# Optimization experiments

Hardware: AMD Instinct MI355X
Metric: run time of the kernel (lower is better)

Reference implementation:

```python
import jax, jax.numpy as jnp
import numpy as np

B, N, OBS, ACT, HID, GD, H = 1024, 64, 128, 16, 256, 64, 4
NEG_SLOPE = 0.2  # GAT leaky-relu alpha


def _gat(x, adj, W, a, concat):
    # x: (B,N,F), W: (H,F,D), a: (H,2D). Equivalent to concat([x_i,x_j]) . a
    # split as x_i.a1 + x_j.a2 -- same math, avoids the (B,H,N,N,2D) tensor.
    D = W.shape[-1]
    xt = jnp.einsum('bnf,hfd->bhnd', x, W)
    si = jnp.einsum('bhnd,hd->bhn', xt, a[:, :D])
    sj = jnp.einsum('bhnd,hd->bhn', xt, a[:, D:])
    s = jax.nn.leaky_relu(si[:, :, :, None] + sj[:, :, None, :], NEG_SLOPE)
    s = jnp.where(adj[:, None, :, :] == 0, -jnp.inf, s)
    w = jax.nn.softmax(s, axis=-1)
    out = jnp.einsum('bhij,bhjd->bhid', w, xt)
    if concat:
        b, n = x.shape[0], x.shape[1]
        return out.transpose(0, 2, 1, 3).reshape(b, n, -1)
    return out.mean(axis=1)


def _mlp3(x, w1, b1, w2, b2, w3, b3):
    # per-agent 3-layer MLP, weights stacked over agent axis n
    h = jax.nn.relu(jnp.einsum('bni,nih->bnh', x, w1) + b1)
    h = jax.nn.relu(jnp.einsum('bnh,nhk->bnk', h, w2) + b2)
    return jnp.einsum('bnk,nko->bno', h, w3) + b3


def _mlp2(x, w1, b1, w2, b2):
    h = jax.nn.relu(jnp.einsum('bni,nih->bnh', x, w1) + b1)
    return jnp.einsum('bnh,nho->bno', h, w2) + b2


def setup_inputs() -> dict:
    key = jax.random.key(0)
    ks = iter(jax.random.split(key, 64))

    def nrm(shape):
        fan_in = shape[-2] if len(shape) >= 2 else shape[-1]
        return jax.random.normal(next(ks), shape, jnp.float32) * np.float32(1.0 / np.sqrt(fan_in))

    AI = OBS + GD   # actor/critic input dim
    CI = OBS + ACT  # SCM / centralized per-agent input dim
    return dict(
        observations=jax.random.normal(next(ks), (B, N, OBS), jnp.float32),
        actions=jax.random.normal(next(ks), (B, N, ACT), jnp.float32),
        adj_matrix=jnp.ones((B, N, N), jnp.float32),
        causal_structure=jnp.eye(OBS, dtype=jnp.float32),
        gat_W=nrm((H, OBS, GD)), gat_a=nrm((H, 2 * GD)),
        cg_W0=nrm((H, OBS, GD)), cg_a0=nrm((H, 2 * GD)),
        cg_W1=nrm((H, H * GD, GD)), cg_a1=nrm((H, 2 * GD)),
        actor_w1=nrm((N, AI, HID)), actor_b1=jnp.zeros((N, HID), jnp.float32),
        actor_w2=nrm((N, HID, HID)), actor_b2=jnp.zeros((N, HID), jnp.float32),
        actor_w3=nrm((N, HID, ACT)), actor_b3=jnp.zeros((N, ACT), jnp.float32),
        critic_w1=nrm((N, AI, HID)), critic_b1=jnp.zeros((N, HID), jnp.float32),
        critic_w2=nrm((N, HID, HID)), critic_b2=jnp.zeros((N, HID), jnp.float32),
        critic_w3=nrm((N, HID, 1)), critic_b3=jnp.zeros((N, 1), jnp.float32),
        cent_w1=nrm((N * CI, HID)), cent_b1=jnp.zeros((HID,), jnp.float32),
        cent_w2=nrm((HID, HID)), cent_b2=jnp.zeros((HID,), jnp.float32),
        cent_w3=nrm((HID, N)), cent_b3=jnp.zeros((N,), jnp.float32),
        scm_causal=jnp.eye(N, dtype=jnp.float32),
        scm_mw1=nrm((N, CI, HID)), scm_mb1=jnp.zeros((N, HID), jnp.float32),
        scm_mw2=nrm((N, HID, HID)), scm_mb2=jnp.zeros((N, HID), jnp.float32),
        scm_mw3=nrm((N, HID, OBS)), scm_mb3=jnp.zeros((N, OBS), jnp.float32),
        scm_nw1=nrm((N, OBS, HID)), scm_nb1=jnp.zeros((N, HID), jnp.float32),
        scm_nw2=nrm((N, HID, OBS)), scm_nb2=jnp.zeros((N, OBS), jnp.float32),
    )


def reference(observations, actions, adj_matrix, causal_structure,
              gat_W, gat_a, cg_W0, cg_a0, cg_W1, cg_a1,
              actor_w1, actor_b1, actor_w2, actor_b2, actor_w3, actor_b3,
              critic_w1, critic_b1, critic_w2, critic_b2, critic_w3, critic_b3,
              cent_w1, cent_b1, cent_w2, cent_b2, cent_w3, cent_b3,
              scm_causal, scm_mw1, scm_mb1, scm_mw2, scm_mb2, scm_mw3, scm_mb3,
              scm_nw1, scm_nb1, scm_nw2, scm_nb2):
    # plain GAT communication features (concat=False -> head mean)
    gat_feat = _gat(observations, adj_matrix, gat_W, gat_a, False)
    # CausalGAT: causal mask on input features, then 2 GAT layers w/ ELU between
    xm = observations @ jax.nn.softmax(causal_structure, axis=-1)
    hcg = jax.nn.elu(_gat(xm, adj_matrix, cg_W0, cg_a0, True))
    causal_feat = _gat(hcg, adj_matrix, cg_W1, cg_a1, False)
    comm = gat_feat + causal_feat
    ai = jnp.concatenate([observations, comm], axis=-1)  # (B,N,OBS+GD)
    actor_out = _mlp3(ai, actor_w1, actor_b1, actor_w2, actor_b2, actor_w3, actor_b3)
    critic_out = _mlp3(ai, critic_w1, critic_b1, critic_w2, critic_b2, critic_w3, critic_b3)
    # centralized critic over flattened (obs, action) of all agents
    flat = jnp.concatenate([observations, actions], axis=-1).reshape(observations.shape[0], -1)
    hc = jax.nn.relu(flat @ cent_w1 + cent_b1)
    hc = jax.nn.relu(hc @ cent_w2 + cent_b2)
    cent_out = hc @ cent_w3 + cent_b3
    # SCM: per-agent causal mechanisms mixed by softmaxed causal matrix + noise model
    cw = jax.nn.softmax(scm_causal, axis=-1)
    combined = jnp.concatenate([observations, actions], axis=-1)
    ce = _mlp3(combined, scm_mw1, scm_mb1, scm_mw2, scm_mb2, scm_mw3, scm_mb3)
    se = jnp.einsum('ij,bjd->bid', cw, ce)
    noise = _mlp2(observations, scm_nw1, scm_nb1, scm_nw2, scm_nb2)
    scm_pred = se + noise
    return (actor_out, critic_out, cent_out, scm_pred)
```

## Files before the change

kernel.cpp:

```cpp
#include <hip/hip_runtime.h>
#include <hip/hip_bf16.h>
#include <math.h>

#define NB 1024
#define NAG 64
#define OBS 128
#define ACTD 16
#define HID 256
#define GD 64
#define NH 4

typedef short bhalf8 __attribute__((ext_vector_type(8)));
typedef float f32x4 __attribute__((ext_vector_type(4)));

__device__ inline unsigned short f2bf_u(float f) {
  __hip_bfloat16 h = __float2bfloat16(f);
  return *(unsigned short*)&h;
}
__device__ inline float bfu2f(unsigned short u) {
  unsigned v = ((unsigned)u) << 16;
  return *(float*)&v;
}
__device__ inline unsigned pk2(float x, float y) {
  float2 f2; f2.x = x; f2.y = y;
  __hip_bfloat162 h = __float22bfloat162_rn(f2);
  return *(unsigned*)&h;
}

__global__ __launch_bounds__(64) void softmax_rows_k(const float* __restrict__ in,
                                                     float* __restrict__ out, int n) {
  int row = blockIdx.x;
  int lane = threadIdx.x;
  const float* r = in + (size_t)row * n;
  float m = -INFINITY;
  for (int j = lane; j < n; j += 64) m = fmaxf(m, r[j]);
#pragma unroll
  for (int off = 32; off; off >>= 1) m = fmaxf(m, __shfl_xor(m, off));
  float s = 0.f;
  for (int j = lane; j < n; j += 64) s += expf(r[j] - m);
#pragma unroll
  for (int off = 32; off; off >>= 1) s += __shfl_xor(s, off);
  float inv = 1.f / s;
  for (int j = lane; j < n; j += 64) out[(size_t)row * n + j] = expf(r[j] - m) * inv;
}

__global__ void cwbf_k(const float* __restrict__ cwsm, unsigned short* __restrict__ cw1,
                       unsigned short* __restrict__ cw2) {
  int idx = blockIdx.x * 256 + threadIdx.x;
  if (idx >= 4096) return;
  float v = cwsm[idx];
  unsigned short hi = f2bf_u(v);
  cw1[idx] = hi;
  cw2[idx] = f2bf_u(v - bfu2f(hi));
}

__global__ __launch_bounds__(256) void transpose_cvt_k(const float* __restrict__ in,
                                                       unsigned short* __restrict__ out,
                                                       int K, int N) {
  __shared__ float t[32][33];
  int k0 = blockIdx.x * 32, n0 = blockIdx.y * 32, z = blockIdx.z;
  int tx = threadIdx.x, ty = threadIdx.y;
  const float* ib = in + (size_t)z * K * N;
  unsigned short* ob = out + (size_t)z * N * K;
#pragma unroll
  for (int i = 0; i < 4; ++i) {
    int k = k0 + ty + 8 * i, n = n0 + tx;
    if (k < K && n < N) t[ty + 8 * i][tx] = ib[(size_t)k * N + n];
  }
  __syncthreads();
#pragma unroll
  for (int i = 0; i < 4; ++i) {
    int n = n0 + ty + 8 * i, k = k0 + tx;
    if (n < N && k < K) ob[(size_t)n * K + k] = f2bf_u(t[tx][ty + 8 * i]);
  }
}

__global__ void repack_wT_k(const float* __restrict__ W, unsigned short* __restrict__ WcT, int F) {
  int idx = blockIdx.x * 256 + threadIdx.x;
  if (idx >= NH * F * 64) return;
  int d = idx & 63;
  int f = (idx >> 6) % F;
  int h = idx / (F * 64);
  WcT[((size_t)(h * 64 + d)) * F + f] = f2bf_u(W[idx]);
}

__global__ __launch_bounds__(256) void gemm_mfma_k(
    const float* __restrict__ A, const unsigned short* __restrict__ BT,
    const float* __restrict__ bias, float* __restrict__ C,
    int M, int N, int K,
    long long lda, long long ldc,
    long long aBS, long long btBS, long long biasBS, long long cBS,
    int act, int kPerSplit) {
  __shared__ unsigned short As[64 * 40];
  __shared__ unsigned short Bs[64 * 40];
  int tid = threadIdx.x;
  int wave = tid >> 6, lane = tid & 63;
  int m0 = blockIdx.x * 64, n0 = blockIdx.y * 64;
  int z = blockIdx.z;
  const float* Ab;
  const unsigned short* Bb;
  const float* biasb = nullptr;
  float* Cb;
  int k_begin, k_end;
  if (kPerSplit > 0) {
    Ab = A; Bb = BT; Cb = C + (long long)z * cBS;
    k_begin = z * kPerSplit;
    k_end = k_begin + kPerSplit;
    if (k_end > K) k_end = K;
  } else {
    Ab = A + (long long)z * aBS;
    Bb = BT + (long long)z * btBS;
    if (bias) biasb = bias + (long long)z * biasBS;
    Cb = C + (long long)z * cBS;
    k_begin = 0; k_end = K;
  }
  int sr = tid >> 2;
  int sk = (tid & 3) * 8;
  int fr = lane & 15;
  int kq = (lane >> 4) * 8;

  f32x4 zf = {0.f, 0.f, 0.f, 0.f};
  f32x4 acc[4] = {zf, zf, zf, zf};

  const unsigned short* bRow = Bb + (long long)(n0 + sr) * K;
  bool bValid = (n0 + sr) < N;
  const float* aRow = Ab + (long long)(m0 + sr) * lda;

  for (int k0 = k_begin; k0 < k_end; k0 += 32) {
    int kk = k0 + sk;
    uint4 aw;
    if (kk + 7 < k_end) {
      const float* ap = aRow + kk;
      float4 v0 = *(const float4*)ap;
      float4 v1 = *(const float4*)(ap + 4);
      aw.x = pk2(v0.x, v0.y); aw.y = pk2(v0.z, v0.w);
      aw.z = pk2(v1.x, v1.y); aw.w = pk2(v1.z, v1.w);
    } else {
      float t[8];
#pragma unroll
      for (int j = 0; j < 8; ++j) t[j] = (kk + j < k_end) ? aRow[kk + j] : 0.f;
      aw.x = pk2(t[0], t[1]); aw.y = pk2(t[2], t[3]);
      aw.z = pk2(t[4], t[5]); aw.w = pk2(t[6], t[7]);
    }
    *(uint4*)&As[sr * 40 + sk] = aw;
    uint4 bw = {0u, 0u, 0u, 0u};
    if (bValid) {
      if (kk + 7 < k_end) {
        bw = *(const uint4*)(bRow + kk);
      } else {
        unsigned short tb[8];
#pragma unroll
        for (int j = 0; j < 8; ++j) tb[j] = (kk + j < k_end) ? bRow[kk + j] : (unsigned short)0;
        bw.x = (unsigned)tb[0] | ((unsigned)tb[1] << 16);
        bw.y = (unsigned)tb[2] | ((unsigned)tb[3] << 16);
        bw.z = (unsigned)tb[4] | ((unsigned)tb[5] << 16);
        bw.w = (unsigned)tb[6] | ((unsigned)tb[7] << 16);
      }
    }
    *(uint4*)&Bs[sr * 40 + sk] = bw;
    __syncthreads();
    bhalf8 af = *(bhalf8*)&As[(16 * wave + fr) * 40 + kq];
#pragma unroll
    for (int t = 0; t < 4; ++t) {
      bhalf8 bf = *(bhalf8*)&Bs[(16 * t + fr) * 40 + kq];
      acc[t] = __builtin_amdgcn_mfma_f32_16x16x32_bf16(af, bf, acc[t], 0, 0, 0);
    }
    __syncthreads();
  }
  int rb = (lane >> 4) * 4;
#pragma unroll
  for (int t = 0; t < 4; ++t) {
    int col = n0 + 16 * t + fr;
    if (col < N) {
      float bv = biasb ? biasb[col] : 0.f;
#pragma unroll
      for (int r = 0; r < 4; ++r) {
        long long row = m0 + 16 * wave + rb + r;
        float v = acc[t][r] + bv;
        if (act == 1) v = fmaxf(v, 0.f);
        Cb[row * ldc + col] = v;
      }
    }
  }
}

__global__ __launch_bounds__(256) void gemm_mfma128_k(
    const float* __restrict__ A, const unsigned short* __restrict__ BT,
    const float* __restrict__ bias, float* __restrict__ C,
    int M, int N, int K,
    long long lda, long long ldc,
    long long aBS, long long btBS, long long biasBS, long long cBS,
    int act, int kPerSplit) {
  __shared__ unsigned short As[128 * 40];
  __shared__ unsigned short Bs[128 * 40];
  int tid = threadIdx.x;
  int wave = tid >> 6, lane = tid & 63;
  int m0 = blockIdx.x * 128, n0 = blockIdx.y * 128;
  int z = blockIdx.z;
  const float* Ab;
  const unsigned short* Bb;
  const float* biasb = nullptr;
  float* Cb;
  int k_begin, k_end;
  if (kPerSplit > 0) {
    Ab = A; Bb = BT; Cb = C + (long long)z * cBS;
    k_begin = z * kPerSplit;
    k_end = k_begin + kPerSplit;
    if (k_end > K) k_end = K;
  } else {
    Ab = A + (long long)z * aBS;
    Bb = BT + (long long)z * btBS;
    if (bias) biasb = bias + (long long)z * biasBS;
    Cb = C + (long long)z * cBS;
    k_begin = 0; k_end = K;
  }
  int sr = tid >> 1;
  int sk = (tid & 1) * 16;
  int mq = (wave >> 1) * 64;
  int nq = (wave & 1) * 64;
  int fr = lane & 15;
  int kq = (lane >> 4) * 8;

  f32x4 zf = {0.f, 0.f, 0.f, 0.f};
  f32x4 acc[4][4];
#pragma unroll
  for (int i = 0; i < 4; ++i)
#pragma unroll
    for (int j = 0; j < 4; ++j) acc[i][j] = zf;

  const float* aRow = Ab + (long long)(m0 + sr) * lda;
  const unsigned short* bRow = Bb + (long long)(n0 + sr) * K;
  bool bValid = (n0 + sr) < N;

  for (int k0 = k_begin; k0 < k_end; k0 += 32) {
    int kk = k0 + sk;
    uint4 aw0, aw1;
    if (kk + 15 < k_end) {
      const float* ap = aRow + kk;
      float4 v0 = *(const float4*)ap;
      float4 v1 = *(const float4*)(ap + 4);
      float4 v2 = *(const float4*)(ap + 8);
      float4 v3 = *(const float4*)(ap + 12);
      aw0.x = pk2(v0.x, v0.y); aw0.y = pk2(v0.z, v0.w);
      aw0.z = pk2(v1.x, v1.y); aw0.w = pk2(v1.z, v1.w);
      aw1.x = pk2(v2.x, v2.y); aw1.y = pk2(v2.z, v2.w);
      aw1.z = pk2(v3.x, v3.y); aw1.w = pk2(v3.z, v3.w);
    } else {
      float t[16];
#pragma unroll
      for (int j = 0; j < 16; ++j) t[j] = (kk + j < k_end) ? aRow[kk + j] : 0.f;
      aw0.x = pk2(t[0], t[1]);   aw0.y = pk2(t[2], t[3]);
      aw0.z = pk2(t[4], t[5]);   aw0.w = pk2(t[6], t[7]);
      aw1.x = pk2(t[8], t[9]);   aw1.y = pk2(t[10], t[11]);
      aw1.z = pk2(t[12], t[13]); aw1.w = pk2(t[14], t[15]);
    }
    *(uint4*)&As[sr * 40 + sk] = aw0;
    *(uint4*)&As[sr * 40 + sk + 8] = aw1;
    uint4 bw0 = {0u, 0u, 0u, 0u}, bw1 = {0u, 0u, 0u, 0u};
    if (bValid) {
      if (kk + 15 < k_end) {
        bw0 = *(const uint4*)(bRow + kk);
        bw1 = *(const uint4*)(bRow + kk + 8);
      } else {
        unsigned short tb[16];
#pragma unroll
        for (int j = 0; j < 16; ++j) tb[j] = (kk + j < k_end) ? bRow[kk + j] : (unsigned short)0;
        bw0.x = (unsigned)tb[0] | ((unsigned)tb[1] << 16);
        bw0.y = (unsigned)tb[2] | ((unsigned)tb[3] << 16);
        bw0.z = (unsigned)tb[4] | ((unsigned)tb[5] << 16);
        bw0.w = (unsigned)tb[6] | ((unsigned)tb[7] << 16);
        bw1.x = (unsigned)tb[8] | ((unsigned)tb[9] << 16);
        bw1.y = (unsigned)tb[10] | ((unsigned)tb[11] << 16);
        bw1.z = (unsigned)tb[12] | ((unsigned)tb[13] << 16);
        bw1.w = (unsigned)tb[14] | ((unsigned)tb[15] << 16);
      }
    }
    *(uint4*)&Bs[sr * 40 + sk] = bw0;
    *(uint4*)&Bs[sr * 40 + sk + 8] = bw1;
    __syncthreads();
    bhalf8 af[4], bf[4];
#pragma unroll
    for (int i = 0; i < 4; ++i) af[i] = *(bhalf8*)&As[(mq + 16 * i + fr) * 40 + kq];
#pragma unroll
    for (int j = 0; j < 4; ++j) bf[j] = *(bhalf8*)&Bs[(nq + 16 * j + fr) * 40 + kq];
#pragma unroll
    for (int i = 0; i < 4; ++i)
#pragma unroll
      for (int j = 0; j < 4; ++j)
        acc[i][j] = __builtin_amdgcn_mfma_f32_16x16x32_bf16(af[i], bf[j], acc[i][j], 0, 0, 0);
    __syncthreads();
  }
  int rb = (lane >> 4) * 4;
#pragma unroll
  for (int j = 0; j < 4; ++j) {
    int col = n0 + nq + 16 * j + fr;
    if (col < N) {
      float bv = biasb ? biasb[col] : 0.f;
#pragma unroll
      for (int i = 0; i < 4; ++i) {
#pragma unroll
        for (int r = 0; r < 4; ++r) {
          long long row = m0 + mq + 16 * i + rb + r;
          float v = acc[i][j][r] + bv;
          if (act == 1) v = fmaxf(v, 0.f);
          Cb[row * ldc + col] = v;
        }
      }
    }
  }
}

__global__ __launch_bounds__(256, 4) void gat_attn4_k(
    const float* __restrict__ xt, const float* __restrict__ a,
    const float* __restrict__ adj, float* __restrict__ out, int mode) {
  int b = blockIdx.x;
  int tid = threadIdx.x;
  int wave = tid >> 6, lane = tid & 63;
  __shared__ unsigned short xT1[64 * 72];
  __shared__ unsigned short xT2[64 * 72];
  __shared__ unsigned short P1[64 * 72];
  __shared__ unsigned short P2[64 * 72];
  __shared__ float si_s[64], sj_s[64];

  const float* adjb = adj + (size_t)b * 4096;
  float adjv[16];
#pragma unroll
  for (int r = 0; r < 16; ++r) adjv[r] = adjb[(size_t)(wave * 16 + r) * 64 + lane];

  int lrow = tid >> 2;
  int cg = tid & 3;
  int fr = lane & 15;
  int kq = (lane >> 4) * 8;
  int ibase = wave * 16;

  bhalf8 ones;
#pragma unroll
  for (int u = 0; u < 8; ++u) ones[u] = (short)0x3F80;

  f32x4 zf = {0.f, 0.f, 0.f, 0.f};
  f32x4 accm[4] = {zf, zf, zf, zf};

  for (int h = 0; h < 4; ++h) {
    const float* xcol = xt + ((size_t)(b * 64 + 16 * wave)) * 256 + h * 64 + lane;
    float v[16];
#pragma unroll
    for (int u = 0; u < 16; ++u) v[u] = xcol[(size_t)u * 256];

    const float* xrow = xt + ((size_t)(b * 64 + lrow)) * 256 + h * 64 + cg * 16;
    const float* ah = a + h * 128;
    float p1 = 0.f, p2 = 0.f;
#pragma unroll
    for (int q = 0; q < 4; ++q) {
      float4 rv = *(const float4*)(xrow + 4 * q);
      int c = cg * 16 + 4 * q;
      p1 += rv.x * ah[c] + rv.y * ah[c + 1] + rv.z * ah[c + 2] + rv.w * ah[c + 3];
      p2 += rv.x * ah[64 + c] + rv.y * ah[64 + c + 1] + rv.z * ah[64 + c + 2] + rv.w * ah[64 + c + 3];
    }
    p1 += __shfl_xor(p1, 1); p1 += __shfl_xor(p1, 2);
    p2 += __shfl_xor(p2, 1); p2 += __shfl_xor(p2, 2);
    if (cg == 0) { si_s[lrow] = p1; sj_s[lrow] = p2; }

    {
      float hf[16];
      uint4 h0, h1, l0, l1;
#pragma unroll
      for (int u = 0; u < 16; ++u) hf[u] = bfu2f(f2bf_u(v[u]));
      h0.x = pk2(hf[0], hf[1]);   h0.y = pk2(hf[2], hf[3]);
      h0.z = pk2(hf[4], hf[5]);   h0.w = pk2(hf[6], hf[7]);
      h1.x = pk2(hf[8], hf[9]);   h1.y = pk2(hf[10], hf[11]);
      h1.z = pk2(hf[12], hf[13]); h1.w = pk2(hf[14], hf[15]);
      l0.x = pk2(v[0] - hf[0], v[1] - hf[1]);     l0.y = pk2(v[2] - hf[2], v[3] - hf[3]);
      l0.z = pk2(v[4] - hf[4], v[5] - hf[5]);     l0.w = pk2(v[6] - hf[6], v[7] - hf[7]);
      l1.x = pk2(v[8] - hf[8], v[9] - hf[9]);     l1.y = pk2(v[10] - hf[10], v[11] - hf[11]);
      l1.z = pk2(v[12] - hf[12], v[13] - hf[13]); l1.w = pk2(v[14] - hf[14], v[15] - hf[15]);
      int base = lane * 72 + 16 * wave;
      *(uint4*)&xT1[base] = h0;
      *(uint4*)&xT1[base + 8] = h1;
      *(uint4*)&xT2[base] = l0;
      *(uint4*)&xT2[base + 8] = l1;
    }
    __syncthreads();

    float sjv = sj_s[lane];
    float maxsj = sjv;
#pragma unroll
    for (int off = 32; off; off >>= 1) maxsj = fmaxf(maxsj, __shfl_xor(maxsj, off));
#pragma unroll
    for (int r = 0; r < 16; ++r) {
      int i = ibase + r;
      float siv = si_s[i];
      float tM = siv + maxsj;
      float Mi = tM > 0.f ? tM : 0.2f * tM;
      float e = siv + sjv;
      e = e > 0.f ? e : 0.2f * e;
      float p = (adjv[r] == 0.f) ? 0.f : expf(e - Mi);
      unsigned short phi = f2bf_u(p);
      P1[i * 72 + lane] = phi;
      P2[i * 72 + lane] = f2bf_u(p - bfu2f(phi));
    }

    bhalf8 a1[2], a2[2];
#pragma unroll
    for (int ks = 0; ks < 2; ++ks) {
      a1[ks] = *(bhalf8*)&P1[(ibase + fr) * 72 + ks * 32 + kq];
      a2[ks] = *(bhalf8*)&P2[(ibase + fr) * 72 + ks * 32 + kq];
    }
    f32x4 accS = zf;
#pragma unroll
    for (int ks = 0; ks < 2; ++ks) {
      accS = __builtin_amdgcn_mfma_f32_16x16x32_bf16(a1[ks], ones, accS, 0, 0, 0);
      accS = __builtin_amdgcn_mfma_f32_16x16x32_bf16(a2[ks], ones, accS, 0, 0, 0);
    }
    f32x4 acc[4] = {zf, zf, zf, zf};
#pragma unroll
    for (int ks = 0; ks < 2; ++ks) {
#pragma unroll
      for (int t = 0; t < 4; ++t) {
        bhalf8 b1 = *(bhalf8*)&xT1[(16 * t + fr) * 72 + ks * 32 + kq];
        bhalf8 b2 = *(bhalf8*)&xT2[(16 * t + fr) * 72 + ks * 32 + kq];
        acc[t] = __builtin_amdgcn_mfma_f32_16x16x32_bf16(a1[ks], b1, acc[t], 0, 0, 0);
        acc[t] = __builtin_amdgcn_mfma_f32_16x16x32_bf16(a1[ks], b2, acc[t], 0, 0, 0);
        acc[t] = __builtin_amdgcn_mfma_f32_16x16x32_bf16(a2[ks], b1, acc[t], 0, 0, 0);
      }
    }
    f32x4 inv;
#pragma unroll
    for (int r = 0; r < 4; ++r) inv[r] = (accS[r] > 0.f) ? 1.f / accS[r] : 0.f;

    int rb = (lane >> 4) * 4;
    if (mode == 2) {
#pragma unroll
      for (int t = 0; t < 4; ++t) {
#pragma unroll
        for (int r = 0; r < 4; ++r) {
          int i = ibase + rb + r;
          float vv = acc[t][r] * inv[r];
          vv = vv > 0.f ? vv : expf(vv) - 1.f;
          out[((size_t)(b * 64 + i)) * 256 + h * 64 + 16 * t + fr] = vv;
        }
      }
    } else {
#pragma unroll
      for (int t = 0; t < 4; ++t)
#pragma unroll
        for (int r = 0; r < 4; ++r) accm[t][r] += 0.25f * acc[t][r] * inv[r];
    }
    __syncthreads();
  }

  if (mode != 2) {
    int rb = (lane >> 4) * 4;
    float* cb = out + (size_t)b * 4096;
#pragma unroll
    for (int t = 0; t < 4; ++t) {
#pragma unroll
      for (int r = 0; r < 4; ++r) {
        int i = ibase + rb + r;
        int col = 16 * t + fr;
        if (mode == 1) cb[i * 64 + col] += accm[t][r];
        else cb[i * 64 + col] = accm[t][r];
      }
    }
  }
}

__global__ void build_ai_k(const float* __restrict__ obs, const float* __restrict__ comm,
                           float* __restrict__ ai) {
  size_t idx = (size_t)blockIdx.x * 256 + threadIdx.x;
  if (idx >= (size_t)NB * NAG * 192) return;
  int c = (int)(idx % 192);
  size_t bn = idx / 192;
  ai[idx] = (c < 128) ? obs[bn * 128 + c] : comm[bn * 64 + (c - 128)];
}

__global__ void build_combined_k(const float* __restrict__ obs, const float* __restrict__ act,
                                 float* __restrict__ cmb) {
  size_t idx = (size_t)blockIdx.x * 256 + threadIdx.x;
  if (idx >= (size_t)NB * NAG * 144) return;
  int c = (int)(idx % 144);
  size_t bn = idx / 144;
  cmb[idx] = (c < 128) ? obs[bn * 128 + c] : act[bn * 16 + (c - 128)];
}

__global__ void reduce_bias_relu_k(const float* __restrict__ part, const float* __restrict__ bias,
                                   float* __restrict__ out) {
  int idx = blockIdx.x * 256 + threadIdx.x;
  float s = 0.f;
#pragma unroll
  for (int zz = 0; zz < 16; ++zz) s += part[(size_t)zz * 262144 + idx];
  s += bias[idx & 255];
  out[idx] = fmaxf(s, 0.f);
}

__global__ __launch_bounds__(256, 4) void se_noise_mfma_k(
    const unsigned short* __restrict__ cw1, const unsigned short* __restrict__ cw2,
    const float* __restrict__ ce, const float* __restrict__ nz,
    float* __restrict__ out) {
  int b = blockIdx.x;
  int tid = threadIdx.x;
  int wave = tid >> 6, lane = tid & 63;
  __shared__ unsigned short xT1[128 * 72];
  __shared__ unsigned short xT2[128 * 72];

  int dd = tid & 127;
  int jh = tid >> 7;
  const float* cecol = ce + (size_t)b * 8192 + dd;
#pragma unroll
  for (int c = 0; c < 2; ++c) {
    int j0 = jh * 32 + c * 16;
    float v[16];
#pragma unroll
    for (int u = 0; u < 16; ++u) v[u] = cecol[(size_t)(j0 + u) * 128];
    float hf[16];
#pragma unroll
    for (int u = 0; u < 16; ++u) hf[u] = bfu2f(f2bf_u(v[u]));
    uint4 h0, h1, l0, l1;
    h0.x = pk2(hf[0], hf[1]);   h0.y = pk2(hf[2], hf[3]);
    h0.z = pk2(hf[4], hf[5]);   h0.w = pk2(hf[6], hf[7]);
    h1.x = pk2(hf[8], hf[9]);   h1.y = pk2(hf[10], hf[11]);
    h1.z = pk2(hf[12], hf[13]); h1.w = pk2(hf[14], hf[15]);
    l0.x = pk2(v[0] - hf[0], v[1] - hf[1]);     l0.y = pk2(v[2] - hf[2], v[3] - hf[3]);
    l0.z = pk2(v[4] - hf[4], v[5] - hf[5]);     l0.w = pk2(v[6] - hf[6], v[7] - hf[7]);
    l1.x = pk2(v[8] - hf[8], v[9] - hf[9]);     l1.y = pk2(v[10] - hf[10], v[11] - hf[11]);
    l1.z = pk2(v[12] - hf[12], v[13] - hf[13]); l1.w = pk2(v[14] - hf[14], v[15] - hf[15]);
    int base = dd * 72 + j0;
    *(uint4*)&xT1[base] = h0;
    *(uint4*)&xT1[base + 8] = h1;
    *(uint4*)&xT2[base] = l0;
    *(uint4*)&xT2[base + 8] = l1;
  }
  __syncthreads();

  int fr = lane & 15;
  int kq = (lane >> 4) * 8;
  int dq = wave * 32;

  bhalf8 bb1[2][2], bb2[2][2];
#pragma unroll
  for (int dt = 0; dt < 2; ++dt)
#pragma unroll
    for (int ks = 0; ks < 2; ++ks) {
      bb1[dt][ks] = *(bhalf8*)&xT1[(dq + dt * 16 + fr) * 72 + ks * 32 + kq];
      bb2[dt][ks] = *(bhalf8*)&xT2[(dq + dt * 16 + fr) * 72 + ks * 32 + kq];
    }

  f32x4 zf = {0.f, 0.f, 0.f, 0.f};
  f32x4 acc[4][2];
#pragma unroll
  for (int it = 0; it < 4; ++it)
#pragma unroll
    for (int dt = 0; dt < 2; ++dt) acc[it][dt] = zf;

#pragma unroll
  for (int it = 0; it < 4; ++it) {
    bhalf8 a1[2], a2[2];
#pragma unroll
    for (int ks = 0; ks < 2; ++ks) {
      a1[ks] = *(const bhalf8*)(cw1 + (it * 16 + fr) * 64 + ks * 32 + kq);
      a2[ks] = *(const bhalf8*)(cw2 + (it * 16 + fr) * 64 + ks * 32 + kq);
    }
#pragma unroll
    for (int dt = 0; dt < 2; ++dt)
#pragma unroll
      for (int ks = 0; ks < 2; ++ks) {
        acc[it][dt] = __builtin_amdgcn_mfma_f32_16x16x32_bf16(a1[ks], bb1[dt][ks], acc[it][dt], 0, 0, 0);
        acc[it][dt] = __builtin_amdgcn_mfma_f32_16x16x32_bf16(a1[ks], bb2[dt][ks], acc[it][dt], 0, 0, 0);
        acc[it][dt] = __builtin_amdgcn_mfma_f32_16x16x32_bf16(a2[ks], bb1[dt][ks], acc[it][dt], 0, 0, 0);
      }
  }

  int rb = (lane >> 4) * 4;
#pragma unroll
  for (int it = 0; it < 4; ++it)
#pragma unroll
    for (int dt = 0; dt < 2; ++dt) {
      int dcol = dq + dt * 16 + fr;
#pragma unroll
      for (int r = 0; r < 4; ++r) {
        int i = it * 16 + rb + r;
        size_t off = (size_t)b * 8192 + (size_t)i * 128 + dcol;
        out[off] = acc[it][dt][r] + nz[off];
      }
    }
}

extern "C" void kernel_launch(void* const* d_in, const int* in_sizes, int n_in,
                              void* d_out, int out_size, void* d_ws, size_t ws_size,
                              hipStream_t stream) {
  (void)in_sizes; (void)n_in; (void)out_size; (void)ws_size;
  const float* obs = (const float*)d_in[0];
  const float* acts = (const float*)d_in[1];
  const float* adj = (const float*)d_in[2];
  const float* causal = (const float*)d_in[3];
  const float* gat_W = (const float*)d_in[4];
  const float* gat_a = (const float*)d_in[5];
  const float* cg_W0 = (const float*)d_in[6];
  const float* cg_a0 = (const float*)d_in[7];
  const float* cg_W1 = (const float*)d_in[8];
  const float* cg_a1 = (const float*)d_in[9];
  const float* aw1 = (const float*)d_in[10]; const float* ab1 = (const float*)d_in[11];
  const float* aw2 = (const float*)d_in[12]; const float* ab2 = (const float*)d_in[13];
  const float* aw3 = (const float*)d_in[14]; const float* ab3 = (const float*)d_in[15];
  const float* crw1 = (const float*)d_in[16]; const float* crb1 = (const float*)d_in[17];
  const float* crw2 = (const float*)d_in[18]; const float* crb2 = (const float*)d_in[19];
  const float* crw3 = (const float*)d_in[20]; const float* crb3 = (const float*)d_in[21];
  const float* cew1 = (const float*)d_in[22]; const float* ceb1 = (const float*)d_in[23];
  const float* cew2 = (const float*)d_in[24]; const float* ceb2 = (const float*)d_in[25];
  const float* cew3 = (const float*)d_in[26]; const float* ceb3 = (const float*)d_in[27];
  const float* scm_causal = (const float*)d_in[28];
  const float* mw1 = (const float*)d_in[29]; const float* mb1 = (const float*)d_in[30];
  const float* mw2 = (const float*)d_in[31]; const float* mb2 = (const float*)d_in[32];
  const float* mw3 = (const float*)d_in[33]; const float* mb3 = (const float*)d_in[34];
  const float* nw1 = (const float*)d_in[35]; const float* nb1 = (const float*)d_in[36];
  const float* nw2 = (const float*)d_in[37]; const float* nb2 = (const float*)d_in[38];

  float* ws = (float*)d_ws;
  float* Ssm  = ws;
  float* cwsm = ws + 16384;
  float* comm = ws + 20480;
  float* AI   = ws + 4214784;
  float* H1   = ws + 16797696;
  float* HCG  = ws + 33574912;
  unsigned short* wbf = (unsigned short*)(ws + 50352128);
  unsigned short* SsmT  = wbf;
  unsigned short* wcT   = wbf + 16384;
  unsigned short* aw1T  = wbf + 81920;
  unsigned short* aw2T  = wbf + 3227648;
  unsigned short* aw3T  = wbf + 7421952;
  unsigned short* crw1T = wbf + 7684096;
  unsigned short* crw2T = wbf + 10829824;
  unsigned short* crw3T = wbf + 15024128;
  unsigned short* cew1T = wbf + 15040512;
  unsigned short* cew2T = wbf + 17399808;
  unsigned short* cew3T = wbf + 17465344;
  unsigned short* mw1T  = wbf + 17481728;
  unsigned short* mw2T  = wbf + 19841024;
  unsigned short* mw3T  = wbf + 24035328;
  unsigned short* nw1T  = wbf + 26132480;
  unsigned short* nw2T  = wbf + 28229632;
  unsigned short* cw1g = (unsigned short*)ws;
  unsigned short* cw2g = cw1g + 4096;

  float* out_actor = (float*)d_out;
  float* out_critic = out_actor + 1048576;
  float* out_cent = out_critic + 65536;
  float* out_scm = out_cent + 65536;

  auto GEMM64 = [&](const float* A, const unsigned short* BT, const float* bias, float* C,
                    int M, int N, int K, long long lda, long long ldc,
                    long long aBS, long long btBS, long long biasBS, long long cBS,
                    int act, int gz, int kPerSplit) {
    dim3 grid(M / 64, (N + 63) / 64, gz);
    hipLaunchKernelGGL(gemm_mfma_k, grid, dim3(256), 0, stream, A, BT, bias, C, M, N, K,
                       lda, ldc, aBS, btBS, biasBS, cBS, act, kPerSplit);
  };
  auto GEMM128 = [&](const float* A, const unsigned short* BT, const float* bias, float* C,
                     int M, int N, int K, long long lda, long long ldc,
                     long long aBS, long long btBS, long long biasBS, long long cBS,
                     int act, int gz, int kPerSplit) {
    dim3 grid(M / 128, (N + 127) / 128, gz);
    hipLaunchKernelGGL(gemm_mfma128_k, grid, dim3(256), 0, stream, A, BT, bias, C, M, N, K,
                       lda, ldc, aBS, btBS, biasBS, cBS, act, kPerSplit);
  };
  auto TRN = [&](const float* in, unsigned short* out, int Z, int K, int N) {
    dim3 grid((K + 31) / 32, (N + 31) / 32, Z);
    hipLaunchKernelGGL(transpose_cvt_k, grid, dim3(32, 8), 0, stream, in, out, K, N);
  };

  hipLaunchKernelGGL(softmax_rows_k, dim3(128), dim3(64), 0, stream, causal, Ssm, 128);
  hipLaunchKernelGGL(softmax_rows_k, dim3(64), dim3(64), 0, stream, scm_causal, cwsm, 64);
  TRN(Ssm, SsmT, 1, 128, 128);
  hipLaunchKernelGGL(cwbf_k, dim3(16), dim3(256), 0, stream, cwsm, cw1g, cw2g);
  TRN(aw1, aw1T, 64, 192, 256);  TRN(aw2, aw2T, 64, 256, 256);  TRN(aw3, aw3T, 64, 256, 16);
  TRN(crw1, crw1T, 64, 192, 256); TRN(crw2, crw2T, 64, 256, 256); TRN(crw3, crw3T, 64, 256, 1);
  TRN(cew1, cew1T, 1, 9216, 256); TRN(cew2, cew2T, 1, 256, 256);  TRN(cew3, cew3T, 1, 256, 64);
  TRN(mw1, mw1T, 64, 144, 256);  TRN(mw2, mw2T, 64, 256, 256);  TRN(mw3, mw3T, 64, 256, 128);
  TRN(nw1, nw1T, 64, 128, 256);  TRN(nw2, nw2T, 64, 256, 128);

  hipLaunchKernelGGL(repack_wT_k, dim3((NH * 128 * 64 + 255) / 256), dim3(256), 0, stream, gat_W, wcT, 128);
  GEMM128(obs, wcT, nullptr, H1, 65536, 256, 128, 128, 256, 0, 0, 0, 0, 0, 1, 0);
  hipLaunchKernelGGL(gat_attn4_k, dim3(1024), dim3(256), 0, stream, H1, gat_a, adj, comm, 0);

  GEMM128(obs, SsmT, nullptr, HCG, 65536, 128, 128, 128, 128, 0, 0, 0, 0, 0, 1, 0);
  hipLaunchKernelGGL(repack_wT_k, dim3((NH * 128 * 64 + 255) / 256), dim3(256), 0, stream, cg_W0, wcT, 128);
  GEMM128(HCG, wcT, nullptr, H1, 65536, 256, 128, 128, 256, 0, 0, 0, 0, 0, 1, 0);
  hipLaunchKernelGGL(gat_attn4_k, dim3(1024), dim3(256), 0, stream, H1, cg_a0, adj, HCG, 2);
  hipLaunchKernelGGL(repack_wT_k, dim3((NH * 256 * 64 + 255) / 256), dim3(256), 0, stream, cg_W1, wcT, 256);
  GEMM128(HCG, wcT, nullptr, H1, 65536, 256, 256, 256, 256, 0, 0, 0, 0, 0, 1, 0);
  hipLaunchKernelGGL(gat_attn4_k, dim3(1024), dim3(256), 0, stream, H1, cg_a1, adj, comm, 1);

  hipLaunchKernelGGL(build_ai_k, dim3((12582912 + 255) / 256), dim3(256), 0, stream, obs, comm, AI);

  GEMM128(AI, aw1T, ab1, H1, 1024, 256, 192, 12288, 16384, 192, 49152, 256, 256, 1, 64, 0);
  GEMM128(H1, aw2T, ab2, HCG, 1024, 256, 256, 16384, 16384, 256, 65536, 256, 256, 1, 64, 0);
  GEMM64(HCG, aw3T, ab3, out_actor, 1024, 16, 256, 16384, 1024, 256, 4096, 16, 16, 0, 64, 0);

  GEMM128(AI, crw1T, crb1, H1, 1024, 256, 192, 12288, 16384, 192, 49152, 256, 256, 1, 64, 0);
  GEMM128(H1, crw2T, crb2, HCG, 1024, 256, 256, 16384, 16384, 256, 65536, 256, 256, 1, 64, 0);
  GEMM64(HCG, crw3T, crb3, out_critic, 1024, 1, 256, 16384, 64, 256, 256, 1, 1, 0, 64, 0);

  hipLaunchKernelGGL(build_combined_k, dim3((9437184 + 255) / 256), dim3(256), 0, stream, obs, acts, AI);
  GEMM128(AI, cew1T, nullptr, H1, 1024, 256, 9216, 9216, 256, 0, 0, 0, 262144, 0, 16, 576);
  hipLaunchKernelGGL(reduce_bias_relu_k, dim3(1024), dim3(256), 0, stream, H1, ceb1, HCG);
  GEMM64(HCG, cew2T, ceb2, H1, 1024, 256, 256, 256, 256, 0, 0, 0, 0, 1, 1, 0);
  GEMM64(H1, cew3T, ceb3, out_cent, 1024, 64, 256, 256, 64, 0, 0, 0, 0, 0, 1, 0);

  GEMM128(AI, mw1T, mb1, H1, 1024, 256, 144, 9216, 16384, 144, 36864, 256, 256, 1, 64, 0);
  GEMM128(H1, mw2T, mb2, HCG, 1024, 256, 256, 16384, 16384, 256, 65536, 256, 256, 1, 64, 0);
  GEMM128(HCG, mw3T, mb3, AI, 1024, 128, 256, 16384, 8192, 256, 32768, 128, 128, 0, 64, 0);

  GEMM128(obs, nw1T, nb1, H1, 1024, 256, 128, 8192, 16384, 128, 32768, 256, 256, 1, 64, 0);
  GEMM128(H1, nw2T, nb2, HCG, 1024, 128, 256, 16384, 8192, 256, 32768, 128, 128, 0, 64, 0);

  hipLaunchKernelGGL(se_noise_mfma_k, dim3(1024), dim3(256), 0, stream, cw1g, cw2g, AI, HCG, out_scm);
}
```

Baseline: 1.007 ms.

## Double-buffer LDS tiles with register prefetch in both MFMA GEMM kernels

Both GEMM kernels now keep two LDS buffers for the A and B tiles. The next K tile is prefetched into registers while MFMAs run on the current buffer, which also removes one __syncthreads per iteration. The aim is to hide global-load latency behind matrix math. In exchange, LDS and register use go up, which may lower occupancy. The 128 kernel also gets a launch_bounds min-blocks hint of 4.

Result: faster. 936.4 us (-7.0%).

```diff
diff --git a/kernel.cpp b/kernel.cpp
--- a/kernel.cpp
+++ b/kernel.cpp
@@ -91,8 +91,8 @@
     long long lda, long long ldc,
     long long aBS, long long btBS, long long biasBS, long long cBS,
     int act, int kPerSplit) {
-  __shared__ unsigned short As[64 * 40];
-  __shared__ unsigned short Bs[64 * 40];
+  __shared__ unsigned short As[2][64 * 40];
+  __shared__ unsigned short Bs[2][64 * 40];
   int tid = threadIdx.x;
   int wave = tid >> 6, lane = tid & 63;
   int m0 = blockIdx.x * 64, n0 = blockIdx.y * 64;
@@ -126,57 +126,73 @@
   bool bValid = (n0 + sr) < N;
   const float* aRow = Ab + (long long)(m0 + sr) * lda;
 
-  for (int k0 = k_begin; k0 < k_end; k0 += 32) {
-    int kk = k0 + sk;
-    uint4 aw;
+  int nt = (k_end - k_begin + 31) / 32;
+
+  float av[8];
+  uint4 bv;
+
+  auto LOADT = [&](int t) {
+    int kk = k_begin + 32 * t + sk;
     if (kk + 7 < k_end) {
       const float* ap = aRow + kk;
-      float4 v0 = *(const float4*)ap;
-      float4 v1 = *(const float4*)(ap + 4);
-      aw.x = pk2(v0.x, v0.y); aw.y = pk2(v0.z, v0.w);
-      aw.z = pk2(v1.x, v1.y); aw.w = pk2(v1.z, v1.w);
+      *(float4*)&av[0] = *(const float4*)ap;
+      *(float4*)&av[4] = *(const float4*)(ap + 4);
     } else {
-      float t[8];
-#pragma unroll
-      for (int j = 0; j < 8; ++j) t[j] = (kk + j < k_end) ? aRow[kk + j] : 0.f;
-      aw.x = pk2(t[0], t[1]); aw.y = pk2(t[2], t[3]);
-      aw.z = pk2(t[4], t[5]); aw.w = pk2(t[6], t[7]);
-    }
-    *(uint4*)&As[sr * 40 + sk] = aw;
-    uint4 bw = {0u, 0u, 0u, 0u};
+#pragma unroll
+      for (int j = 0; j < 8; ++j) av[j] = (kk + j < k_end) ? aRow[kk + j] : 0.f;
+    }
+    bv.x = bv.y = bv.z = bv.w = 0u;
     if (bValid) {
       if (kk + 7 < k_end) {
-        bw = *(const uint4*)(bRow + kk);
+        bv = *(const uint4*)(bRow + kk);
       } else {
         unsigned short tb[8];
 #pragma unroll
         for (int j = 0; j < 8; ++j) tb[j] = (kk + j < k_end) ? bRow[kk + j] : (unsigned short)0;
-        bw.x = (unsigned)tb[0] | ((unsigned)tb[1] << 16);
-        bw.y = (unsigned)tb[2] | ((unsigned)tb[3] << 16);
-        bw.z = (unsigned)tb[4] | ((unsigned)tb[5] << 16);
-        bw.w = (unsigned)tb[6] | ((unsigned)tb[7] << 16);
-      }
-    }
-    *(uint4*)&Bs[sr * 40 + sk] = bw;
-    __syncthreads();
-    bhalf8 af = *(bhalf8*)&As[(16 * wave + fr) * 40 + kq];
-#pragma unroll
-    for (int t = 0; t < 4; ++t) {
-      bhalf8 bf = *(bhalf8*)&Bs[(16 * t + fr) * 40 + kq];
-      acc[t] = __builtin_amdgcn_mfma_f32_16x16x32_bf16(af, bf, acc[t], 0, 0, 0);
-    }
-    __syncthreads();
+        bv.x = (unsigned)tb[0] | ((unsigned)tb[1] << 16);
+        bv.y = (unsigned)tb[2] | ((unsigned)tb[3] << 16);
+        bv.z = (unsigned)tb[4] | ((unsigned)tb[5] << 16);
+        bv.w = (unsigned)tb[6] | ((unsigned)tb[7] << 16);
+      }
+    }
+  };
+  auto STORE = [&](int buf) {
+    uint4 aw;
+    aw.x = pk2(av[0], av[1]); aw.y = pk2(av[2], av[3]);
+    aw.z = pk2(av[4], av[5]); aw.w = pk2(av[6], av[7]);
+    *(uint4*)&As[buf][sr * 40 + sk] = aw;
+    *(uint4*)&Bs[buf][sr * 40 + sk] = bv;
+  };
+
+  LOADT(0);
+  STORE(0);
+  if (nt > 1) LOADT(1);
+  __syncthreads();
+
+  for (int t = 0; t < nt; ++t) {
+    int cur = t & 1;
+    if (t + 1 < nt) {
+      STORE(cur ^ 1);
+      if (t + 2 < nt) LOADT(t + 2);
+    }
+    bhalf8 af = *(bhalf8*)&As[cur][(16 * wave + fr) * 40 + kq];
+#pragma unroll
+    for (int t4 = 0; t4 < 4; ++t4) {
+      bhalf8 bf = *(bhalf8*)&Bs[cur][(16 * t4 + fr) * 40 + kq];
+      acc[t4] = __builtin_amdgcn_mfma_f32_16x16x32_bf16(af, bf, acc[t4], 0, 0, 0);
+    }
+    if (t + 1 < nt) __syncthreads();
   }
   int rb = (lane >> 4) * 4;
 #pragma unroll
   for (int t = 0; t < 4; ++t) {
     int col = n0 + 16 * t + fr;
     if (col < N) {
-      float bv = biasb ? biasb[col] : 0.f;
+      float bv2 = biasb ? biasb[col] : 0.f;
 #pragma unroll
       for (int r = 0; r < 4; ++r) {
         long long row = m0 + 16 * wave + rb + r;
-        float v = acc[t][r] + bv;
+        float v = acc[t][r] + bv2;
         if (act == 1) v = fmaxf(v, 0.f);
         Cb[row * ldc + col] = v;
       }
@@ -184,15 +200,15 @@
   }
 }
 
-__global__ __launch_bounds__(256) void gemm_mfma128_k(
+__global__ __launch_bounds__(256, 4) void gemm_mfma128_k(
     const float* __restrict__ A, const unsigned short* __restrict__ BT,
     const float* __restrict__ bias, float* __restrict__ C,
     int M, int N, int K,
     long long lda, long long ldc,
     long long aBS, long long btBS, long long biasBS, long long cBS,
     int act, int kPerSplit) {
-  __shared__ unsigned short As[128 * 40];
-  __shared__ unsigned short Bs[128 * 40];
+  __shared__ unsigned short As[2][128 * 40];
+  __shared__ unsigned short Bs[2][128 * 40];
   int tid = threadIdx.x;
   int wave = tid >> 6, lane = tid & 63;
   int m0 = blockIdx.x * 128, n0 = blockIdx.y * 128;
@@ -232,76 +248,91 @@
   const unsigned short* bRow = Bb + (long long)(n0 + sr) * K;
   bool bValid = (n0 + sr) < N;
 
-  for (int k0 = k_begin; k0 < k_end; k0 += 32) {
-    int kk = k0 + sk;
-    uint4 aw0, aw1;
+  int nt = (k_end - k_begin + 31) / 32;
+
+  float av[16];
+  uint4 bv0, bv1;
+
+  auto LOADT = [&](int t) {
+    int kk = k_begin + 32 * t + sk;
     if (kk + 15 < k_end) {
       const float* ap = aRow + kk;
-      float4 v0 = *(const float4*)ap;
-      float4 v1 = *(const float4*)(ap + 4);
-      float4 v2 = *(const float4*)(ap + 8);
-      float4 v3 = *(const float4*)(ap + 12);
-      aw0.x = pk2(v0.x, v0.y); aw0.y = pk2(v0.z, v0.w);
-      aw0.z = pk2(v1.x, v1.y); aw0.w = pk2(v1.z, v1.w);
-      aw1.x = pk2(v2.x, v2.y); aw1.y = pk2(v2.z, v2.w);
-      aw1.z = pk2(v3.x, v3.y); aw1.w = pk2(v3.z, v3.w);
+      *(float4*)&av[0]  = *(const float4*)ap;
+      *(float4*)&av[4]  = *(const float4*)(ap + 4);
+      *(float4*)&av[8]  = *(const float4*)(ap + 8);
+      *(float4*)&av[12] = *(const float4*)(ap + 12);
     } else {
-      float t[16];
-#pragma unroll
-      for (int j = 0; j < 16; ++j) t[j] = (kk + j < k_end) ? aRow[kk + j] : 0.f;
-      aw0.x = pk2(t[0], t[1]);   aw0.y = pk2(t[2], t[3]);
-      aw0.z = pk2(t[4], t[5]);   aw0.w = pk2(t[6], t[7]);
-      aw1.x = pk2(t[8], t[9]);   aw1.y = pk2(t[10], t[11]);
-      aw1.z = pk2(t[12], t[13]); aw1.w = pk2(t[14], t[15]);
-    }
-    *(uint4*)&As[sr * 40 + sk] = aw0;
-    *(uint4*)&As[sr * 40 + sk + 8] = aw1;
-    uint4 bw0 = {0u, 0u, 0u, 0u}, bw1 = {0u, 0u, 0u, 0u};
+#pragma unroll
+      for (int j = 0; j < 16; ++j) av[j] = (kk + j < k_end) ? aRow[kk + j] : 0.f;
+    }
+    bv0.x = bv0.y = bv0.z = bv0.w = 0u;
+    bv1.x = bv1.y = bv1.z = bv1.w = 0u;
     if (bValid) {
       if (kk + 15 < k_end) {
-        bw0 = *(const uint4*)(bRow + kk);
-        bw1 = *(const uint4*)(bRow + kk + 8);
+        bv0 = *(const uint4*)(bRow + kk);
+        bv1 = *(const uint4*)(bRow + kk + 8);
       } else {
         unsigned short tb[16];
 #pragma unroll
         for (int j = 0; j < 16; ++j) tb[j] = (kk + j < k_end) ? bRow[kk + j] : (unsigned short)0;
-        bw0.x = (unsigned)tb[0] | ((unsigned)tb[1] << 16);
-        bw0.y = (unsigned)tb[2] | ((unsigned)tb[3] << 16);
-        bw0.z = (unsigned)tb[4] | ((unsigned)tb[5] << 16);
-        bw0.w = (unsigned)tb[6] | ((unsigned)tb[7] << 16);
-        bw1.x = (unsigned)tb[8] | ((unsigned)tb[9] << 16);
-        bw1.y = (unsigned)tb[10] | ((unsigned)tb[11] << 16);
-        bw1.z = (unsigned)tb[12] | ((unsigned)tb[13] << 16);
-        bw1.w = (unsigned)tb[14] | ((unsigned)tb[15] << 16);
-      }
-    }
-    *(uint4*)&Bs[sr * 40 + sk] = bw0;
-    *(uint4*)&Bs[sr * 40 + sk + 8] = bw1;
-    __syncthreads();
+        bv0.x = (unsigned)tb[0] | ((unsigned)tb[1] << 16);
+        bv0.y = (unsigned)tb[2] | ((unsigned)tb[3] << 16);
+        bv0.z = (unsigned)tb[4] | ((unsigned)tb[5] << 16);
+        bv0.w = (unsigned)tb[6] | ((unsigned)tb[7] << 16);
+        bv1.x = (unsigned)tb[8] | ((unsigned)tb[9] << 16);
+        bv1.y = (unsigned)tb[10] | ((unsigned)tb[11] << 16);
+        bv1.z = (unsigned)tb[12] | ((unsigned)tb[13] << 16);
+        bv1.w = (unsigned)tb[14] | ((unsigned)tb[15] << 16);
+      }
+    }
+  };
+  auto STORE = [&](int buf) {
+    uint4 aw0, aw1;
+    aw0.x = pk2(av[0], av[1]);   aw0.y = pk2(av[2], av[3]);
+    aw0.z = pk2(av[4], av[5]);   aw0.w = pk2(av[6], av[7]);
+    aw1.x = pk2(av[8], av[9]);   aw1.y = pk2(av[10], av[11]);
+    aw1.z = pk2(av[12], av[13]); aw1.w = pk2(av[14], av[15]);
+    *(uint4*)&As[buf][sr * 40 + sk] = aw0;
+    *(uint4*)&As[buf][sr * 40 + sk + 8] = aw1;
+    *(uint4*)&Bs[buf][sr * 40 + sk] = bv0;
+    *(uint4*)&Bs[buf][sr * 40 + sk + 8] = bv1;
+  };
+
+  LOADT(0);
+  STORE(0);
+  if (nt > 1) LOADT(1);
+  __syncthreads();
+
+  for (int t = 0; t < nt; ++t) {
+    int cur = t & 1;
+    if (t + 1 < nt) {
+      STORE(cur ^ 1);
+      if (t + 2 < nt) LOADT(t + 2);
+    }
     bhalf8 af[4], bf[4];
 #pragma unroll
-    for (int i = 0; i < 4; ++i) af[i] = *(bhalf8*)&As[(mq + 16 * i + fr) * 40 + kq];
-#pragma unroll
-    for (int j = 0; j < 4; ++j) bf[j] = *(bhalf8*)&Bs[(nq + 16 * j + fr) * 40 + kq];
+    for (int i = 0; i < 4; ++i) af[i] = *(bhalf8*)&As[cur][(mq + 16 * i + fr) * 40 + kq];
+#pragma unroll
+    for (int j = 0; j < 4; ++j) bf[j] = *(bhalf8*)&Bs[cur][(nq + 16 * j + fr) * 40 + kq];
 #pragma unroll
     for (int i = 0; i < 4; ++i)
 #pragma unroll
       for (int j = 0; j < 4; ++j)
         acc[i][j] = __builtin_amdgcn_mfma_f32_16x16x32_bf16(af[i], bf[j], acc[i][j], 0, 0, 0);
-    __syncthreads();
+    if (t + 1 < nt) __syncthreads();
   }
   int rb = (lane >> 4) * 4;
 #pragma unroll
   for (int j = 0; j < 4; ++j) {
     int col = n0 + nq + 16 * j + fr;
     if (col < N) {
-      float bv = biasb ? biasb[col] : 0.f;
+      float bv2 = biasb ? biasb[col] : 0.f;
 #pragma unroll
       for (int i = 0; i < 4; ++i) {
 #pragma unroll
         for (int r = 0; r < 4; ++r) {
           long long row = m0 + mq + 16 * i + rb + r;
-          float v = acc[i][j][r] + bv;
+          float v = acc[i][j][r] + bv2;
           if (act == 1) v = fmaxf(v, 0.f);
           Cb[row * ldc + col] = v;
         }
```
